# Performance work log

Hardware: AMD Instinct MI355X
Metric: run time of the kernel (lower is better)

## Reference

```python
import jax, jax.numpy as jnp
import numpy as np

ALPHA = 0.2          # LeakyReLU negative slope
NEG_INF = -9e15      # mask value from the original code


def setup_inputs() -> dict:
    key = jax.random.key(0)
    k1, k2, k3, k4 = jax.random.split(key, 4)
    B, N, F_in, F_out = 8, 2048, 64, 64
    x = jax.random.normal(k1, (B, N, F_in), dtype=jnp.float32)
    adj = jax.random.randint(k2, (B, N, N), 0, 2, dtype=jnp.int32)
    W = jax.random.normal(k3, (F_in, F_out), dtype=jnp.float32)
    a = jax.random.normal(k4, (2 * F_out, 1), dtype=jnp.float32)
    return {"x": x, "adj": adj, "W": W, "a": a}


def reference(x, adj, W, a):
    # h: [B, N, F_out]
    h = jnp.matmul(x, W)
    F_out = W.shape[1]
    a1 = a[:F_out, 0]   # source half of attention vector
    a2 = a[F_out:, 0]   # target half
    # e_ij = leakyrelu(h_i . a1 + h_j . a2)  -- identical math to the
    # original cat([h_i, h_j]) @ a without materializing [B,N*N,2F].
    s1 = jnp.einsum('bnf,f->bn', h, a1)  # [B, N]
    s2 = jnp.einsum('bnf,f->bn', h, a2)  # [B, N]
    e = jax.nn.leaky_relu(s1[:, :, None] + s2[:, None, :], negative_slope=ALPHA)
    masked = jnp.where(adj > 0, e, NEG_INF)
    attention = jax.nn.softmax(masked, axis=2)  # [B, N, N]
    # dropout p=0.0 / eval mode -> identity
    h_prime = jnp.matmul(attention, h)          # [B, N, F_out]
    return jax.nn.elu(h_prime)                  # concat=True branch
```

## Files before the change

kernel.cpp:

```cpp
#include <hip/hip_runtime.h>
#include <cstdint>

#define LRELU_ALPHA 0.2f
#define NEG_INF -9000000000000000.0f
#define L2E 1.4426950408889634f

typedef __bf16 bf16x8 __attribute__((ext_vector_type(8)));
typedef float floatx4 __attribute__((ext_vector_type(4)));
typedef unsigned int uintx4 __attribute__((ext_vector_type(4)));

constexpr int Bb = 8, Nn = 2048, Ff = 64;
constexpr int TJ = 64;
constexpr int SEGW = 8;
constexpr int SLICE = Nn / SEGW;
constexpr int NT = SLICE / TJ;
constexpr int NROWS = Bb * Nn;
constexpr int MCH = Nn / 64;

__device__ __forceinline__ unsigned short f2bf(float f) {
    unsigned u = __builtin_bit_cast(unsigned, f);
    u = u + 0x7FFFu + ((u >> 16) & 1u);
    return (unsigned short)(u >> 16);
}

__device__ __forceinline__ unsigned cvt_pk_bf16(float lo, float hi) {
    unsigned r;
    asm("v_cvt_pk_bf16_f32 %0, %1, %2" : "=v"(r) : "v"(lo), "v"(hi));
    return r;
}

__global__ __launch_bounds__(256) void gat_pack(
    const int* __restrict__ adj, unsigned long long* __restrict__ masks)
{
    const int wid  = blockIdx.x * 4 + (threadIdx.x >> 6);
    const int lane = threadIdx.x & 63;
    #pragma unroll
    for (int rr = 0; rr < 2; ++rr) {
        const int row = wid * 2 + rr;
        const int* ar = adj + (size_t)row * Nn;
        unsigned long long acc = 0;
        #pragma unroll
        for (int cb = 0; cb < 8; ++cb) {
            int v0 = ar[(cb * 4 + 0) * 64 + lane];
            int v1 = ar[(cb * 4 + 1) * 64 + lane];
            int v2 = ar[(cb * 4 + 2) * 64 + lane];
            int v3 = ar[(cb * 4 + 3) * 64 + lane];
            unsigned long long m0 = __ballot(v0 > 0);
            unsigned long long m1 = __ballot(v1 > 0);
            unsigned long long m2 = __ballot(v2 > 0);
            unsigned long long m3 = __ballot(v3 > 0);
            if (lane == cb * 4 + 0) acc = m0;
            if (lane == cb * 4 + 1) acc = m1;
            if (lane == cb * 4 + 2) acc = m2;
            if (lane == cb * 4 + 3) acc = m3;
        }
        if (lane < 32) masks[(size_t)row * MCH + lane] = acc;
    }
}

__global__ __launch_bounds__(256) void gat_prep(
    const float* __restrict__ x, const float* __restrict__ W, const float* __restrict__ a,
    unsigned short* __restrict__ hT, float* __restrict__ s1g, float* __restrict__ s2g)
{
    constexpr int STR2 = 36;
    __shared__ unsigned short hblk[64 * STR2];
    const int tid = threadIdx.x;
    const int blk = blockIdx.x;
    const int b  = blk >> 6;
    const int i0 = (blk & 63) * 32;
    const int w    = tid >> 6;
    const int lane = tid & 63;

    float wcol[64];
    #pragma unroll
    for (int k = 0; k < 64; ++k) wcol[k] = W[k * 64 + lane];
    const float a1 = a[lane], a2 = a[64 + lane];

    for (int r = 0; r < 8; ++r) {
        const int il = w * 8 + r;
        const int i  = i0 + il;
        const float* xrow = x + ((size_t)(b * Nn + i)) * 64;
        float h0 = 0.f, h1 = 0.f, h2 = 0.f, h3 = 0.f;
        #pragma unroll
        for (int k = 0; k < 64; k += 4) {
            h0 = fmaf(xrow[k],     wcol[k],     h0);
            h1 = fmaf(xrow[k + 1], wcol[k + 1], h1);
            h2 = fmaf(xrow[k + 2], wcol[k + 2], h2);
            h3 = fmaf(xrow[k + 3], wcol[k + 3], h3);
        }
        const float h = (h0 + h1) + (h2 + h3);
        float p1 = h * a1, p2 = h * a2;
        #pragma unroll
        for (int off = 32; off; off >>= 1) {
            p1 += __shfl_xor(p1, off);
            p2 += __shfl_xor(p2, off);
        }
        if (lane == 0) { s1g[b * Nn + i] = p1; s2g[b * Nn + i] = p2; }
        hblk[lane * STR2 + il] = f2bf(h);
    }
    __syncthreads();
    {
        const int f = tid >> 2, c = (tid & 3) * 8;
        uint4 v = *reinterpret_cast<const uint4*>(&hblk[f * STR2 + c]);
        *reinterpret_cast<uint4*>(hT + ((size_t)b * 64 + f) * Nn + i0 + c) = v;
    }
}

__global__ __launch_bounds__(512, 4) void gat_attn(
    const unsigned long long* __restrict__ masks, const unsigned short* __restrict__ hT,
    const float* __restrict__ s1g, const float* __restrict__ s2g,
    float* __restrict__ out)
{
    __shared__ float O_lds[SEGW][16][65];
    __shared__ float m_lds[SEGW][16];
    __shared__ float l_lds[SEGW][16];

    const int tid  = threadIdx.x;
    const int blk  = blockIdx.x;
    const int b    = blk >> 7;
    const int i0   = (blk & 127) * 16;
    const int s    = tid >> 6;
    const int lane = tid & 63;
    const int fl   = lane & 15;
    const int q    = lane >> 4;

    const int i = i0 + fl;
    const float s1v = s1g[b * Nn + i];
    const unsigned short* hTb = hT + (size_t)b * 64 * Nn + s * SLICE;
    const float* s2b = s2g + b * Nn + s * SLICE;
    const unsigned long long* mrow = masks + (size_t)(b * Nn + i) * MCH + s * NT;

    float m = NEG_INF, l = 0.f;
    floatx4 C[4] = {};

    unsigned long long mk = mrow[0];
    float4 sA = *reinterpret_cast<const float4*>(&s2b[q * 8]);
    float4 sB = *reinterpret_cast<const float4*>(&s2b[q * 8 + 4]);
    float4 sC = *reinterpret_cast<const float4*>(&s2b[32 + q * 8]);
    float4 sD = *reinterpret_cast<const float4*>(&s2b[32 + q * 8 + 4]);

    #pragma unroll
    for (int jt = 0; jt < NT; ++jt) {
        const int jloc = jt * TJ;

        bf16x8 Bv[8];
        #pragma unroll
        for (int u = 0; u < 4; ++u) {
            Bv[2 * u] = *reinterpret_cast<const bf16x8*>(
                hTb + (size_t)(u * 16 + fl) * Nn + jloc + q * 8);
            Bv[2 * u + 1] = *reinterpret_cast<const bf16x8*>(
                hTb + (size_t)(u * 16 + fl) * Nn + jloc + 32 + q * 8);
        }

        const int jn = (jt + 1 < NT) ? jloc + TJ : jloc;
        const unsigned long long mk_n = mrow[(jt + 1 < NT) ? jt + 1 : jt];
        float4 nA = *reinterpret_cast<const float4*>(&s2b[jn + q * 8]);
        float4 nB = *reinterpret_cast<const float4*>(&s2b[jn + q * 8 + 4]);
        float4 nC = *reinterpret_cast<const float4*>(&s2b[jn + 32 + q * 8]);
        float4 nD = *reinterpret_cast<const float4*>(&s2b[jn + 32 + q * 8 + 4]);

        const unsigned blo = ((unsigned)mk >> (q * 8)) & 0xFFu;
        const unsigned bhi = ((unsigned)(mk >> 32) >> (q * 8)) & 0xFFu;
        float p[16];
        {
            const float s2v0[8] = { sA.x, sA.y, sA.z, sA.w, sB.x, sB.y, sB.z, sB.w };
            const float s2v1[8] = { sC.x, sC.y, sC.z, sC.w, sD.x, sD.y, sD.z, sD.w };
            #pragma unroll
            for (int jj = 0; jj < 8; ++jj) {
                float ev = s1v + s2v0[jj];
                ev = fmaxf(ev, LRELU_ALPHA * ev);
                p[jj] = (blo & (1u << jj)) ? ev : NEG_INF;
            }
            #pragma unroll
            for (int jj = 0; jj < 8; ++jj) {
                float ev = s1v + s2v1[jj];
                ev = fmaxf(ev, LRELU_ALPHA * ev);
                p[8 + jj] = (bhi & (1u << jj)) ? ev : NEG_INF;
            }
        }

        float tmax = p[0];
        #pragma unroll
        for (int k = 1; k < 16; ++k) tmax = fmaxf(tmax, p[k]);
        tmax = fmaxf(tmax, __shfl_xor(tmax, 16));
        tmax = fmaxf(tmax, __shfl_xor(tmax, 32));
        const float m_new = fmaxf(m, tmax);

        if (__any(m_new > m)) {
            const float alpha_s = exp2f((m - m_new) * L2E);
            l *= alpha_s;
            float ac[4];
            #pragma unroll
            for (int r = 0; r < 4; ++r) ac[r] = __shfl(alpha_s, q * 4 + r);
            #pragma unroll
            for (int u = 0; u < 4; ++u)
                #pragma unroll
                for (int r = 0; r < 4; ++r) C[u][r] *= ac[r];
            m = m_new;
        }

        float tsum = 0.f;
        #pragma unroll
        for (int k = 0; k < 16; ++k) {
            p[k] = exp2f((p[k] - m) * L2E);
            tsum += p[k];
        }
        tsum += __shfl_xor(tsum, 16);
        tsum += __shfl_xor(tsum, 32);
        l += tsum;

        uintx4 pa, pb;
        #pragma unroll
        for (int d = 0; d < 4; ++d) {
            pa[d] = cvt_pk_bf16(p[2 * d],     p[2 * d + 1]);
            pb[d] = cvt_pk_bf16(p[8 + 2 * d], p[8 + 2 * d + 1]);
        }
        const bf16x8 A0 = __builtin_bit_cast(bf16x8, pa);
        const bf16x8 A1 = __builtin_bit_cast(bf16x8, pb);

        __builtin_amdgcn_s_setprio(1);
        #pragma unroll
        for (int u = 0; u < 4; ++u) {
            C[u] = __builtin_amdgcn_mfma_f32_16x16x32_bf16(A0, Bv[2 * u],     C[u], 0, 0, 0);
            C[u] = __builtin_amdgcn_mfma_f32_16x16x32_bf16(A1, Bv[2 * u + 1], C[u], 0, 0, 0);
        }
        __builtin_amdgcn_s_setprio(0);

        mk = mk_n; sA = nA; sB = nB; sC = nC; sD = nD;
    }

    #pragma unroll
    for (int u = 0; u < 4; ++u)
        #pragma unroll
        for (int r = 0; r < 4; ++r)
            O_lds[s][q * 4 + r][u * 16 + fl] = C[u][r];
    if (q == 0) { m_lds[s][fl] = m; l_lds[s][fl] = l; }
    __syncthreads();

    const int row = tid >> 5;
    const int f0  = (tid & 31) * 2;

    float mv[SEGW];
    #pragma unroll
    for (int k = 0; k < SEGW; ++k) mv[k] = m_lds[k][row];
    float mstar = mv[0];
    #pragma unroll
    for (int k = 1; k < SEGW; ++k) mstar = fmaxf(mstar, mv[k]);

    float lsum = 0.f, acc0 = 0.f, acc1 = 0.f;
    #pragma unroll
    for (int k = 0; k < SEGW; ++k) {
        const float wgt = exp2f((mv[k] - mstar) * L2E);
        lsum += l_lds[k][row] * wgt;
        const float2 ov = *reinterpret_cast<const float2*>(&O_lds[k][row][f0]);
        acc0 += ov.x * wgt;
        acc1 += ov.y * wgt;
    }
    const float inv = 1.f / lsum;
    float v0 = acc0 * inv, v1 = acc1 * inv;
    v0 = (v0 > 0.f) ? v0 : (exp2f(v0 * L2E) - 1.f);
    v1 = (v1 > 0.f) ? v1 : (exp2f(v1 * L2E) - 1.f);
    float2 o2; o2.x = v0; o2.y = v1;
    *reinterpret_cast<float2*>(&out[((size_t)(b * Nn + i0 + row)) * 64 + f0]) = o2;
}

extern "C" void kernel_launch(void* const* d_in, const int* in_sizes, int n_in,
                              void* d_out, int out_size, void* d_ws, size_t ws_size,
                              hipStream_t stream) {
    const float* x   = (const float*)d_in[0];
    const int*   adj = (const int*)d_in[1];
    const float* W   = (const float*)d_in[2];
    const float* a   = (const float*)d_in[3];
    float* out = (float*)d_out;

    char* p = (char*)d_ws;
    unsigned short* hT = (unsigned short*)p;  p += (size_t)Bb * 64 * Nn * sizeof(unsigned short);
    float* s1 = (float*)p;                    p += (size_t)NROWS * sizeof(float);
    float* s2 = (float*)p;                    p += (size_t)NROWS * sizeof(float);
    unsigned long long* masks = (unsigned long long*)p;

    gat_pack<<<dim3(NROWS / 8), dim3(256), 0, stream>>>(adj, masks);
    gat_prep<<<dim3(Bb * Nn / 32), dim3(256), 0, stream>>>(x, W, a, hT, s1, s2);
    gat_attn<<<dim3(NROWS / 16), dim3(512), 0, stream>>>(masks, hT, s1, s2, out);
}
```

Measured before the change: 253.5 us.

## Precompute exact row max in pack kernel, drop online softmax rescaling

The adjacency pack kernel now runs after the prep kernel. While packing it computes each row's exact masked maximum of s2 and turns it into the row's true softmax max, using the fact that LeakyReLU is monotonic. The attention kernel then uses this fixed max, which removes the per-tile max reduction, cross-lane shuffles, conditional accumulator rescaling and the cross-segment max merge. It also drops the software prefetch of the next tile's mask and s2 values, and the pack kernel now reads s2 alongside adj.

Result: slower. 271.4 us (+7.1%).

```diff
diff --git a/kernel.cpp b/kernel.cpp
--- a/kernel.cpp
+++ b/kernel.cpp
@@ -27,35 +27,6 @@
     unsigned r;
     asm("v_cvt_pk_bf16_f32 %0, %1, %2" : "=v"(r) : "v"(lo), "v"(hi));
     return r;
-}
-
-__global__ __launch_bounds__(256) void gat_pack(
-    const int* __restrict__ adj, unsigned long long* __restrict__ masks)
-{
-    const int wid  = blockIdx.x * 4 + (threadIdx.x >> 6);
-    const int lane = threadIdx.x & 63;
-    #pragma unroll
-    for (int rr = 0; rr < 2; ++rr) {
-        const int row = wid * 2 + rr;
-        const int* ar = adj + (size_t)row * Nn;
-        unsigned long long acc = 0;
-        #pragma unroll
-        for (int cb = 0; cb < 8; ++cb) {
-            int v0 = ar[(cb * 4 + 0) * 64 + lane];
-            int v1 = ar[(cb * 4 + 1) * 64 + lane];
-            int v2 = ar[(cb * 4 + 2) * 64 + lane];
-            int v3 = ar[(cb * 4 + 3) * 64 + lane];
-            unsigned long long m0 = __ballot(v0 > 0);
-            unsigned long long m1 = __ballot(v1 > 0);
-            unsigned long long m2 = __ballot(v2 > 0);
-            unsigned long long m3 = __ballot(v3 > 0);
-            if (lane == cb * 4 + 0) acc = m0;
-            if (lane == cb * 4 + 1) acc = m1;
-            if (lane == cb * 4 + 2) acc = m2;
-            if (lane == cb * 4 + 3) acc = m3;
-        }
-        if (lane < 32) masks[(size_t)row * MCH + lane] = acc;
-    }
 }
 
 __global__ __launch_bounds__(256) void gat_prep(
@@ -106,13 +77,44 @@
     }
 }
 
+__global__ __launch_bounds__(256) void gat_pack(
+    const int* __restrict__ adj, const float* __restrict__ s1g, const float* __restrict__ s2g,
+    unsigned long long* __restrict__ masks, float* __restrict__ row_m)
+{
+    const int wid  = blockIdx.x * 4 + (threadIdx.x >> 6);
+    const int lane = threadIdx.x & 63;
+    #pragma unroll
+    for (int rr = 0; rr < 2; ++rr) {
+        const int row = wid * 2 + rr;
+        const int b   = row >> 11;
+        const int* ar = adj + (size_t)row * Nn;
+        const float* s2r = s2g + (size_t)b * Nn;
+        unsigned long long acc = 0;
+        float mx = NEG_INF;
+        #pragma unroll
+        for (int cb = 0; cb < MCH; ++cb) {
+            const int   v  = ar[cb * 64 + lane];
+            const float sv = s2r[cb * 64 + lane];
+            const unsigned long long mb = __ballot(v > 0);
+            if (lane == cb) acc = mb;
+            mx = (v > 0) ? fmaxf(mx, sv) : mx;
+        }
+        #pragma unroll
+        for (int off = 32; off; off >>= 1) mx = fmaxf(mx, __shfl_xor(mx, off));
+        if (lane < 32) masks[(size_t)row * MCH + lane] = acc;
+        if (lane == 0) {
+            const float ev = s1g[row] + mx;
+            row_m[row] = fmaxf(ev, LRELU_ALPHA * ev);
+        }
+    }
+}
+
 __global__ __launch_bounds__(512, 4) void gat_attn(
     const unsigned long long* __restrict__ masks, const unsigned short* __restrict__ hT,
     const float* __restrict__ s1g, const float* __restrict__ s2g,
-    float* __restrict__ out)
+    const float* __restrict__ row_m, float* __restrict__ out)
 {
     __shared__ float O_lds[SEGW][16][65];
-    __shared__ float m_lds[SEGW][16];
     __shared__ float l_lds[SEGW][16];
 
     const int tid  = threadIdx.x;
@@ -126,22 +128,23 @@
 
     const int i = i0 + fl;
     const float s1v = s1g[b * Nn + i];
+    const float ci  = -row_m[b * Nn + i] * L2E;
     const unsigned short* hTb = hT + (size_t)b * 64 * Nn + s * SLICE;
     const float* s2b = s2g + b * Nn + s * SLICE;
     const unsigned long long* mrow = masks + (size_t)(b * Nn + i) * MCH + s * NT;
 
-    float m = NEG_INF, l = 0.f;
+    float l = 0.f;
     floatx4 C[4] = {};
-
-    unsigned long long mk = mrow[0];
-    float4 sA = *reinterpret_cast<const float4*>(&s2b[q * 8]);
-    float4 sB = *reinterpret_cast<const float4*>(&s2b[q * 8 + 4]);
-    float4 sC = *reinterpret_cast<const float4*>(&s2b[32 + q * 8]);
-    float4 sD = *reinterpret_cast<const float4*>(&s2b[32 + q * 8 + 4]);
 
     #pragma unroll
     for (int jt = 0; jt < NT; ++jt) {
         const int jloc = jt * TJ;
+
+        const unsigned long long mk = mrow[jt];
+        const float4 sA = *reinterpret_cast<const float4*>(&s2b[jloc + q * 8]);
+        const float4 sB = *reinterpret_cast<const float4*>(&s2b[jloc + q * 8 + 4]);
+        const float4 sC = *reinterpret_cast<const float4*>(&s2b[jloc + 32 + q * 8]);
+        const float4 sD = *reinterpret_cast<const float4*>(&s2b[jloc + 32 + q * 8 + 4]);
 
         bf16x8 Bv[8];
         #pragma unroll
@@ -152,15 +155,9 @@
                 hTb + (size_t)(u * 16 + fl) * Nn + jloc + 32 + q * 8);
         }
 
-        const int jn = (jt + 1 < NT) ? jloc + TJ : jloc;
-        const unsigned long long mk_n = mrow[(jt + 1 < NT) ? jt + 1 : jt];
-        float4 nA = *reinterpret_cast<const float4*>(&s2b[jn + q * 8]);
-        float4 nB = *reinterpret_cast<const float4*>(&s2b[jn + q * 8 + 4]);
-        float4 nC = *reinterpret_cast<const float4*>(&s2b[jn + 32 + q * 8]);
-        float4 nD = *reinterpret_cast<const float4*>(&s2b[jn + 32 + q * 8 + 4]);
-
-        const unsigned blo = ((unsigned)mk >> (q * 8)) & 0xFFu;
-        const unsigned bhi = ((unsigned)(mk >> 32) >> (q * 8)) & 0xFFu;
+        const unsigned blo = ((unsigned)(mk >> (q * 8))) & 0xFFu;
+        const unsigned bhi = ((unsigned)(mk >> (32 + q * 8))) & 0xFFu;
+
         float p[16];
         {
             const float s2v0[8] = { sA.x, sA.y, sA.z, sA.w, sB.x, sB.y, sB.z, sB.w };
@@ -169,45 +166,19 @@
             for (int jj = 0; jj < 8; ++jj) {
                 float ev = s1v + s2v0[jj];
                 ev = fmaxf(ev, LRELU_ALPHA * ev);
-                p[jj] = (blo & (1u << jj)) ? ev : NEG_INF;
+                const float t = exp2f(fmaf(ev, L2E, ci));
+                p[jj] = (blo & (1u << jj)) ? t : 0.f;
+                l += p[jj];
             }
             #pragma unroll
             for (int jj = 0; jj < 8; ++jj) {
                 float ev = s1v + s2v1[jj];
                 ev = fmaxf(ev, LRELU_ALPHA * ev);
-                p[8 + jj] = (bhi & (1u << jj)) ? ev : NEG_INF;
+                const float t = exp2f(fmaf(ev, L2E, ci));
+                p[8 + jj] = (bhi & (1u << jj)) ? t : 0.f;
+                l += p[8 + jj];
             }
         }
-
-        float tmax = p[0];
-        #pragma unroll
-        for (int k = 1; k < 16; ++k) tmax = fmaxf(tmax, p[k]);
-        tmax = fmaxf(tmax, __shfl_xor(tmax, 16));
-        tmax = fmaxf(tmax, __shfl_xor(tmax, 32));
-        const float m_new = fmaxf(m, tmax);
-
-        if (__any(m_new > m)) {
-            const float alpha_s = exp2f((m - m_new) * L2E);
-            l *= alpha_s;
-            float ac[4];
-            #pragma unroll
-            for (int r = 0; r < 4; ++r) ac[r] = __shfl(alpha_s, q * 4 + r);
-            #pragma unroll
-            for (int u = 0; u < 4; ++u)
-                #pragma unroll
-                for (int r = 0; r < 4; ++r) C[u][r] *= ac[r];
-            m = m_new;
-        }
-
-        float tsum = 0.f;
-        #pragma unroll
-        for (int k = 0; k < 16; ++k) {
-            p[k] = exp2f((p[k] - m) * L2E);
-            tsum += p[k];
-        }
-        tsum += __shfl_xor(tsum, 16);
-        tsum += __shfl_xor(tsum, 32);
-        l += tsum;
 
         uintx4 pa, pb;
         #pragma unroll
@@ -225,36 +196,29 @@
             C[u] = __builtin_amdgcn_mfma_f32_16x16x32_bf16(A1, Bv[2 * u + 1], C[u], 0, 0, 0);
         }
         __builtin_amdgcn_s_setprio(0);
-
-        mk = mk_n; sA = nA; sB = nB; sC = nC; sD = nD;
-    }
+    }
+
+    l += __shfl_xor(l, 16);
+    l += __shfl_xor(l, 32);
 
     #pragma unroll
     for (int u = 0; u < 4; ++u)
         #pragma unroll
         for (int r = 0; r < 4; ++r)
             O_lds[s][q * 4 + r][u * 16 + fl] = C[u][r];
-    if (q == 0) { m_lds[s][fl] = m; l_lds[s][fl] = l; }
+    if (q == 0) l_lds[s][fl] = l;
     __syncthreads();
 
     const int row = tid >> 5;
     const int f0  = (tid & 31) * 2;
 
-    float mv[SEGW];
-    #pragma unroll
-    for (int k = 0; k < SEGW; ++k) mv[k] = m_lds[k][row];
-    float mstar = mv[0];
-    #pragma unroll
-    for (int k = 1; k < SEGW; ++k) mstar = fmaxf(mstar, mv[k]);
-
     float lsum = 0.f, acc0 = 0.f, acc1 = 0.f;
     #pragma unroll
     for (int k = 0; k < SEGW; ++k) {
-        const float wgt = exp2f((mv[k] - mstar) * L2E);
-        lsum += l_lds[k][row] * wgt;
+        lsum += l_lds[k][row];
         const float2 ov = *reinterpret_cast<const float2*>(&O_lds[k][row][f0]);
-        acc0 += ov.x * wgt;
-        acc1 += ov.y * wgt;
+        acc0 += ov.x;
+        acc1 += ov.y;
     }
     const float inv = 1.f / lsum;
     float v0 = acc0 * inv, v1 = acc1 * inv;
@@ -278,8 +242,10 @@
     float* s1 = (float*)p;                    p += (size_t)NROWS * sizeof(float);
     float* s2 = (float*)p;                    p += (size_t)NROWS * sizeof(float);
     unsigned long long* masks = (unsigned long long*)p;
-
-    gat_pack<<<dim3(NROWS / 8), dim3(256), 0, stream>>>(adj, masks);
+    p += (size_t)NROWS * MCH * sizeof(unsigned long long);
+    float* row_m = (float*)p;
+
     gat_prep<<<dim3(Bb * Nn / 32), dim3(256), 0, stream>>>(x, W, a, hT, s1, s2);
-    gat_attn<<<dim3(NROWS / 16), dim3(512), 0, stream>>>(masks, hT, s1, s2, out);
-}
+    gat_pack<<<dim3(NROWS / 8), dim3(256), 0, stream>>>(adj, s1, s2, masks, row_m);
+    gat_attn<<<dim3(NROWS / 16), dim3(512), 0, stream>>>(masks, hT, s1, s2, row_m, out);
+}
```
